# Kernel optimization log

Measured on AMD Instinct MI355X. Metric: run time of the kernel, lower is better.

Reference implementation:

```python
import jax, jax.numpy as jnp
import numpy as np

N = 50000      # nodes
E = 800000     # edges (before self loops)
IN = 128       # in_channels
HID = 128      # 2*out_channels
OUT = 64       # out_channels
NEG_SLOPE = 0.2


def _gat_conv(x, src, dst, W, a_src, a_dst, b, n_nodes):
    """Single-head PyG GATConv (concat=True, heads=1, self-loops already added)."""
    h = x @ W                                   # [N, F]
    alpha_s = h @ a_src                         # [N]
    alpha_d = h @ a_dst                         # [N]
    e = alpha_s[src] + alpha_d[dst]             # [E'] logits per edge j->i
    e = jnp.where(e > 0, e, NEG_SLOPE * e)      # LeakyReLU(0.2)
    # segment softmax over destination node
    m = jax.ops.segment_max(e, dst, num_segments=n_nodes)   # [N]
    w = jnp.exp(e - m[dst])                                   # [E']
    denom = jax.ops.segment_sum(w, dst, num_segments=n_nodes) # [N]
    alpha = w / denom[dst]                                     # [E']
    out = jax.ops.segment_sum(alpha[:, None] * h[src], dst, num_segments=n_nodes)
    return out + b


def _with_self_loops(edge_index, n_nodes):
    loop = jnp.arange(n_nodes, dtype=edge_index.dtype)
    src = jnp.concatenate([edge_index[0], loop])
    dst = jnp.concatenate([edge_index[1], loop])
    return src, dst


def setup_inputs() -> dict:
    key = jax.random.key(0)
    ks = jax.random.split(key, 10)
    s = 0.1
    return {
        "x": jax.random.normal(ks[0], (N, IN), jnp.float32),
        "edge_index": jax.random.randint(ks[1], (2, E), 0, N, jnp.int32),
        "W1": jax.random.normal(ks[2], (IN, HID), jnp.float32) * s,
        "a1_src": jax.random.normal(ks[3], (HID,), jnp.float32) * s,
        "a1_dst": jax.random.normal(ks[4], (HID,), jnp.float32) * s,
        "b1": jnp.zeros((HID,), jnp.float32),
        "W2": jax.random.normal(ks[5], (HID, OUT), jnp.float32) * s,
        "a2_src": jax.random.normal(ks[6], (OUT,), jnp.float32) * s,
        "a2_dst": jax.random.normal(ks[7], (OUT,), jnp.float32) * s,
        "b2": jnp.zeros((OUT,), jnp.float32),
    }


def reference(x, edge_index, W1, a1_src, a1_dst, b1, W2, a2_src, a2_dst, b2):
    src, dst = _with_self_loops(edge_index, N)
    h = _gat_conv(x, src, dst, W1, a1_src, a1_dst, b1, N)
    h = jax.nn.relu(h)
    return _gat_conv(h, src, dst, W2, a2_src, a2_dst, b2, N)
```

## Files before the change

kernel.cpp:

```cpp
#include <hip/hip_runtime.h>
#include <hip/hip_bf16.h>


#define BCAP 4096

typedef __attribute__((ext_vector_type(8))) short bf16x8;
typedef __attribute__((ext_vector_type(4))) float f32x4;

__device__ __forceinline__ unsigned short bf16bits(float f){
  __hip_bfloat16 b = __float2bfloat16(f);
  return *(unsigned short*)&b;
}
__device__ __forceinline__ float bf16lo(unsigned int v){ return __uint_as_float(v << 16); }
__device__ __forceinline__ float bf16hi(unsigned int v){ return __uint_as_float(v & 0xFFFF0000u); }

__global__ void init_k(int* bucketCount, float* as1, float* ad1, float* as2, float* ad2, int n){
  int i = blockIdx.x*blockDim.x + threadIdx.x;
  if (i < 512) bucketCount[i] = 0;
  if (i < n){ as1[i]=0.f; ad1[i]=0.f; as2[i]=0.f; ad2[i]=0.f; }
}

__global__ void prep_w(const float* __restrict__ W, unsigned short* __restrict__ Wt,
                       int K, int NC){
  int idx = blockIdx.x*blockDim.x + threadIdx.x;
  int total = NC*K/2;
  if (idx < total){
    int n = idx / (K/2), k2 = idx % (K/2);
    float a = W[(size_t)(2*k2)*NC + n];
    float b = W[(size_t)(2*k2+1)*NC + n];
    ushort2 o; o.x = bf16bits(a); o.y = bf16bits(b);
    *(ushort2*)&Wt[(size_t)n*K + 2*k2] = o;
  }
}

__global__ __launch_bounds__(256) void bucket_scatter(
    const int* __restrict__ src, const int* __restrict__ dst,
    int* __restrict__ bucketCount, unsigned int* __restrict__ gbuf, int E)
{
  __shared__ int hist[512];
  __shared__ int base[512];
  int t = threadIdx.x;
  int e0 = blockIdx.x * 2048;
  hist[t] = 0; hist[t+256] = 0;
  __syncthreads();
  int sv[8], dv[8];
  #pragma unroll
  for (int k=0;k<8;k++){
    int i = e0 + t + k*256;
    if (i < E){ sv[k]=src[i]; dv[k]=dst[i]; atomicAdd(&hist[dv[k]>>7], 1); }
    else { sv[k] = -1; dv[k] = 0; }
  }
  __syncthreads();
  int h0 = hist[t], h1 = hist[t+256];
  if (h0 > 0) base[t]     = atomicAdd(&bucketCount[t],     h0);
  if (h1 > 0) base[t+256] = atomicAdd(&bucketCount[t+256], h1);
  __syncthreads();
  hist[t] = 0; hist[t+256] = 0;
  __syncthreads();
  #pragma unroll
  for (int k=0;k<8;k++){
    if (sv[k] >= 0){
      int b = dv[k] >> 7;
      int r = base[b] + atomicAdd(&hist[b], 1);
      if (r < BCAP)
        gbuf[(size_t)b*BCAP + r] = ((unsigned)(dv[k] & 127) << 16) | (unsigned)sv[k];
    }
  }
}

__global__ void bucket_scan(const int* __restrict__ bucketCount,
                            int* __restrict__ bucketBase, int* __restrict__ offs,
                            int N, int E, int B){
  __shared__ int sh[512];
  int t = threadIdx.x;
  int nd = 0;
  if (t < B){ int lo = t*128; nd = (N - lo < 128) ? (N - lo) : 128; }
  int v = (t < B ? bucketCount[t] : 0) + nd;
  sh[t] = v;
  __syncthreads();
  for (int d=1; d<512; d<<=1){
    int x = (t >= d) ? sh[t-d] : 0;
    __syncthreads();
    sh[t] += x;
    __syncthreads();
  }
  if (t < B) bucketBase[t] = sh[t] - v;
  if (t == 0) offs[N] = E + N;
}

__global__ __launch_bounds__(256) void fine_sort(
    const unsigned int* __restrict__ gbuf, const int* __restrict__ bucketCount,
    const int* __restrict__ bucketBase, int* __restrict__ offs,
    int* __restrict__ srcS, int N)
{
  __shared__ int h[128];
  __shared__ int pre[128];
  __shared__ int rank[128];
  int b = blockIdx.x, t = threadIdx.x;
  int cnt = bucketCount[b]; if (cnt > BCAP) cnt = BCAP;
  int lo = b*128;
  int nd = (N - lo < 128) ? (N - lo) : 128;
  int base = bucketBase[b];
  if (t < 128){ h[t] = 0; rank[t] = 0; }
  __syncthreads();
  for (int i = t; i < cnt; i += 256)
    atomicAdd(&h[(gbuf[(size_t)b*BCAP + i] >> 16) & 127], 1);
  __syncthreads();
  if (t < 128) pre[t] = (t < nd) ? (h[t] + 1) : 0;
  __syncthreads();
  for (int d=1; d<128; d<<=1){
    int x = (t >= d && t < 128) ? pre[t-d] : 0;
    __syncthreads();
    if (t < 128) pre[t] += x;
    __syncthreads();
  }
  int seg = (t < nd) ? (h[t] + 1) : 0;
  int ex  = (t < 128) ? (pre[t] - seg) : 0;
  if (t < nd){
    offs[lo + t] = base + ex;
    srcS[base + ex] = lo + t;
  }
  __syncthreads();
  if (t < 128) pre[t] = ex;
  __syncthreads();
  for (int i = t; i < cnt; i += 256){
    unsigned e = gbuf[(size_t)b*BCAP + i];
    int dl = (e >> 16) & 127;
    int s  = e & 0xFFFF;
    int r  = atomicAdd(&rank[dl], 1);
    srcS[base + pre[dl] + 1 + r] = s;
  }
}

template<typename AT, int NC>
__global__ __launch_bounds__(256) void gemm_mfma(
    const AT* __restrict__ A, const unsigned short* __restrict__ Wt,
    const float* __restrict__ avs, const float* __restrict__ avd,
    unsigned short* __restrict__ H,
    float* __restrict__ as_, float* __restrict__ ad_, int M)
{
  const int K = 128;
  __shared__ unsigned short As[64*136];
  __shared__ unsigned short Ws[NC*136];
  int t = threadIdx.x;
  int rowBase = blockIdx.x * 64;

  if (sizeof(AT) == 4){
    const float* Af = (const float*)A;
    #pragma unroll
    for (int i=0;i<8;i++){
      int idx = t + i*256; int r = idx>>5, k4 = idx&31;
      int grow = rowBase + r;
      float4 v = (grow<M) ? *(const float4*)&Af[(size_t)grow*K + k4*4]
                          : make_float4(0.f,0.f,0.f,0.f);
      ushort4 o; o.x=bf16bits(v.x); o.y=bf16bits(v.y); o.z=bf16bits(v.z); o.w=bf16bits(v.w);
      *(ushort4*)&As[r*136 + k4*4] = o;
    }
  } else {
    const unsigned short* Ah = (const unsigned short*)A;
    #pragma unroll
    for (int i=0;i<4;i++){
      int idx = t + i*256; int r = idx>>4, k8 = idx&15;
      int grow = rowBase + r;
      uint4 v = (grow<M) ? *(const uint4*)&Ah[(size_t)grow*K + k8*8]
                         : make_uint4(0u,0u,0u,0u);
      *(uint4*)&As[r*136 + k8*8] = v;
    }
  }
  #pragma unroll
  for (int i=0;i<NC/16;i++){
    int idx = t + i*256; int n = idx>>4, k8 = idx&15;
    *(uint4*)&Ws[n*136 + k8*8] = *(const uint4*)&Wt[(size_t)n*K + k8*8];
  }
  __syncthreads();

  int wave = t>>6, lane = t&63, ln = lane&15, q = lane>>4;
  f32x4 acc[NC/16];
  #pragma unroll
  for (int nt=0; nt<NC/16; nt++) acc[nt] = (f32x4){0.f,0.f,0.f,0.f};
  #pragma unroll
  for (int kk=0;kk<4;kk++){
    bf16x8 a = *(const bf16x8*)&As[(wave*16+ln)*136 + kk*32 + q*8];
    #pragma unroll
    for (int nt=0; nt<NC/16; nt++){
      bf16x8 b = *(const bf16x8*)&Ws[(nt*16+ln)*136 + kk*32 + q*8];
      acc[nt] = __builtin_amdgcn_mfma_f32_16x16x32_bf16(a, b, acc[nt], 0, 0, 0);
    }
  }

  float asl[NC/16], adl[NC/16];
  #pragma unroll
  for (int nt=0; nt<NC/16; nt++){ asl[nt]=avs[nt*16+ln]; adl[nt]=avd[nt*16+ln]; }
  #pragma unroll
  for (int i=0;i<4;i++){
    int grow = rowBase + wave*16 + q*4 + i;
    if (grow < M){
      float ps=0.f, pd=0.f;
      #pragma unroll
      for (int nt=0; nt<NC/16; nt++){
        float v = acc[nt][i];
        H[(size_t)grow*NC + nt*16 + ln] = bf16bits(v);
        ps += v*asl[nt]; pd += v*adl[nt];
      }
      #pragma unroll
      for (int d=1; d<16; d<<=1){ ps += __shfl_xor(ps,d); pd += __shfl_xor(pd,d); }
      if (ln==0){ atomicAdd(&as_[grow], ps); atomicAdd(&ad_[grow], pd); }
    }
  }
}

template<bool RELU>
__global__ __launch_bounds__(256) void edge_agg128(
    const int* __restrict__ offs, const int* __restrict__ srcS,
    const float* __restrict__ asrc, const float* __restrict__ adst,
    const unsigned short* __restrict__ Hin, const float* __restrict__ bias,
    unsigned short* __restrict__ outp, int n)
{
  int wid  = (blockIdx.x * 256 + threadIdx.x) >> 6;
  int lane = threadIdx.x & 63;
  if (wid >= n) return;
  int beg = offs[wid], end = offs[wid+1];
  float ad = adst[wid];
  int qw = lane >> 4, ql = lane & 15;
  float acc[8] = {}; float denom = 0.f;
  for (int base = beg; base < end; base += 64){
    int m = end - base; if (m > 64) m = 64;
    int   sv = (lane < m) ? srcS[base + lane] : 0;
    float av = (lane < m) ? asrc[sv] : 0.f;
    float ev = av + ad;
    ev = (ev > 0.f) ? ev : 0.2f*ev;
    float wv = (lane < m) ? __expf(ev) : 0.f;
    for (int j = 0; j < m; j += 4){
      int idx = j + qw;
      int   s = __shfl(sv, idx);
      float w = __shfl(wv, idx);
      uint4 hv = *(const uint4*)&Hin[(size_t)s*128 + ql*8];
      denom += w;
      acc[0]+=w*bf16lo(hv.x); acc[1]+=w*bf16hi(hv.x);
      acc[2]+=w*bf16lo(hv.y); acc[3]+=w*bf16hi(hv.y);
      acc[4]+=w*bf16lo(hv.z); acc[5]+=w*bf16hi(hv.z);
      acc[6]+=w*bf16lo(hv.w); acc[7]+=w*bf16hi(hv.w);
    }
  }
  denom += __shfl_xor(denom,16); denom += __shfl_xor(denom,32);
  #pragma unroll
  for (int k=0;k<8;k++){ acc[k]+=__shfl_xor(acc[k],16); acc[k]+=__shfl_xor(acc[k],32); }
  if (qw == 0){
    float inv = 1.0f / denom;
    unsigned short o[8];
    #pragma unroll
    for (int k=0;k<8;k++){
      float v = acc[k]*inv + bias[ql*8+k];
      if (RELU) v = fmaxf(v, 0.f);
      o[k] = bf16bits(v);
    }
    *(uint4*)&outp[(size_t)wid*128 + ql*8] = *(uint4*)o;
  }
}

__global__ __launch_bounds__(256) void edge_agg64(
    const int* __restrict__ offs, const int* __restrict__ srcS,
    const float* __restrict__ asrc, const float* __restrict__ adst,
    const unsigned short* __restrict__ Hin, const float* __restrict__ bias,
    float* __restrict__ outp, int n)
{
  int wid  = (blockIdx.x * 256 + threadIdx.x) >> 6;
  int lane = threadIdx.x & 63;
  if (wid >= n) return;
  int beg = offs[wid], end = offs[wid+1];
  float ad = adst[wid];
  int ew = lane >> 3, el = lane & 7;
  float acc[8] = {}; float denom = 0.f;
  for (int base = beg; base < end; base += 64){
    int m = end - base; if (m > 64) m = 64;
    int   sv = (lane < m) ? srcS[base + lane] : 0;
    float av = (lane < m) ? asrc[sv] : 0.f;
    float ev = av + ad;
    ev = (ev > 0.f) ? ev : 0.2f*ev;
    float wv = (lane < m) ? __expf(ev) : 0.f;
    for (int j = 0; j < m; j += 8){
      int idx = j + ew;
      int   s = __shfl(sv, idx);
      float w = __shfl(wv, idx);
      uint4 hv = *(const uint4*)&Hin[(size_t)s*64 + el*8];
      denom += w;
      acc[0]+=w*bf16lo(hv.x); acc[1]+=w*bf16hi(hv.x);
      acc[2]+=w*bf16lo(hv.y); acc[3]+=w*bf16hi(hv.y);
      acc[4]+=w*bf16lo(hv.z); acc[5]+=w*bf16hi(hv.z);
      acc[6]+=w*bf16lo(hv.w); acc[7]+=w*bf16hi(hv.w);
    }
  }
  denom += __shfl_xor(denom,8); denom += __shfl_xor(denom,16); denom += __shfl_xor(denom,32);
  #pragma unroll
  for (int k=0;k<8;k++){
    acc[k]+=__shfl_xor(acc[k],8); acc[k]+=__shfl_xor(acc[k],16); acc[k]+=__shfl_xor(acc[k],32);
  }
  if (ew == 0){
    float inv = 1.0f / denom;
    float4 o0, o1;
    o0.x = acc[0]*inv + bias[el*8+0]; o0.y = acc[1]*inv + bias[el*8+1];
    o0.z = acc[2]*inv + bias[el*8+2]; o0.w = acc[3]*inv + bias[el*8+3];
    o1.x = acc[4]*inv + bias[el*8+4]; o1.y = acc[5]*inv + bias[el*8+5];
    o1.z = acc[6]*inv + bias[el*8+6]; o1.w = acc[7]*inv + bias[el*8+7];
    *(float4*)&outp[(size_t)wid*64 + el*8]     = o0;
    *(float4*)&outp[(size_t)wid*64 + el*8 + 4] = o1;
  }
}

extern "C" void kernel_launch(void* const* d_in, const int* in_sizes, int n_in,
                              void* d_out, int out_size, void* d_ws, size_t ws_size,
                              hipStream_t stream) {
  const int IN = 128, HID = 128, OUT = 64;
  const int N = in_sizes[0] / IN;
  const int E = in_sizes[1] / 2;
  const int B = (N + 127) / 128;

  const float* x    = (const float*)d_in[0];
  const int*   ei   = (const int*)d_in[1];
  const float* W1   = (const float*)d_in[2];
  const float* a1s  = (const float*)d_in[3];
  const float* a1d  = (const float*)d_in[4];
  const float* b1   = (const float*)d_in[5];
  const float* W2   = (const float*)d_in[6];
  const float* a2s  = (const float*)d_in[7];
  const float* a2d  = (const float*)d_in[8];
  const float* b2   = (const float*)d_in[9];
  float* out = (float*)d_out;

  char* w = (char*)d_ws;
  unsigned short* W1t = (unsigned short*)w; w += (size_t)HID*IN*2;
  unsigned short* W2t = (unsigned short*)w; w += (size_t)OUT*HID*2;
  unsigned short* h1    = (unsigned short*)w; w += (size_t)N*128*2;
  unsigned short* hrelu = (unsigned short*)w; w += (size_t)N*128*2;
  unsigned short* h2 = h1;
  float* as1   = (float*)w; w += (size_t)N*4;
  float* ad1   = (float*)w; w += (size_t)N*4;
  float* as2   = (float*)w; w += (size_t)N*4;
  float* ad2   = (float*)w; w += (size_t)N*4;
  int* offs    = (int*)w;   w += (size_t)(N+1)*4;
  int* bucketCount = (int*)w; w += 512*4;
  int* bucketBase  = (int*)w; w += 512*4;
  int* srcS    = (int*)w;   w += (size_t)(E+N)*4;
  unsigned int* gbuf = (unsigned int*)w; w += (size_t)B*BCAP*4;

  const int* esrc = ei;
  const int* edst = ei + E;

  hipLaunchKernelGGL(init_k,  dim3((N+255)/256), dim3(256), 0, stream,
                     bucketCount, as1, ad1, as2, ad2, N);
  hipLaunchKernelGGL(prep_w, dim3((HID*IN/2+255)/256), dim3(256), 0, stream, W1, W1t, IN, HID);
  hipLaunchKernelGGL(prep_w, dim3((OUT*HID/2+255)/256), dim3(256), 0, stream, W2, W2t, HID, OUT);
  hipLaunchKernelGGL(bucket_scatter, dim3((E+2047)/2048), dim3(256), 0, stream,
                     esrc, edst, bucketCount, gbuf, E);
  hipLaunchKernelGGL(bucket_scan, dim3(1), dim3(512), 0, stream,
                     bucketCount, bucketBase, offs, N, E, B);
  hipLaunchKernelGGL(fine_sort, dim3(B), dim3(256), 0, stream,
                     gbuf, bucketCount, bucketBase, offs, srcS, N);

  hipLaunchKernelGGL((gemm_mfma<float,128>), dim3((N+63)/64), dim3(256), 0, stream,
                     x, W1t, a1s, a1d, h1, as1, ad1, N);
  hipLaunchKernelGGL((edge_agg128<true>), dim3((N*64+255)/256), dim3(256), 0, stream,
                     offs, srcS, as1, ad1, h1, b1, hrelu, N);
  hipLaunchKernelGGL((gemm_mfma<unsigned short,64>), dim3((N+63)/64), dim3(256), 0, stream,
                     hrelu, W2t, a2s, a2d, h2, as2, ad2, N);
  hipLaunchKernelGGL(edge_agg64, dim3((N*64+255)/256), dim3(256), 0, stream,
                     offs, srcS, as2, ad2, h2, b2, out, N);
}
```

Measured before the change: 208.7 us.

## Fuse bucket scatter with layer-1 GEMM, fold scan into sort, precompute W2·a2

The edge bucket scatter and the first GEMM now run in one launch, with blocks split by index, so the memory-bound scatter and the MFMA GEMM can overlap. The bucket prefix scan is recomputed redundantly inside each fine_sort block, which removes a single-block launch. The layer-2 attention logits are computed in the layer-1 aggregation epilogue from precomputed W2·a2 vectors, so the second GEMM drops its atomics. Zero-initialisation moves to memsets. In exchange, the logits are taken from fp32 pre-rounding values rather than bf16 H, and each sort block repeats the 512-wide scan.

```diff
diff --git a/kernel.cpp b/kernel.cpp
--- a/kernel.cpp
+++ b/kernel.cpp
@@ -14,139 +14,50 @@
 __device__ __forceinline__ float bf16lo(unsigned int v){ return __uint_as_float(v << 16); }
 __device__ __forceinline__ float bf16hi(unsigned int v){ return __uint_as_float(v & 0xFFFF0000u); }
 
-__global__ void init_k(int* bucketCount, float* as1, float* ad1, float* as2, float* ad2, int n){
-  int i = blockIdx.x*blockDim.x + threadIdx.x;
-  if (i < 512) bucketCount[i] = 0;
-  if (i < n){ as1[i]=0.f; ad1[i]=0.f; as2[i]=0.f; ad2[i]=0.f; }
-}
-
-__global__ void prep_w(const float* __restrict__ W, unsigned short* __restrict__ Wt,
-                       int K, int NC){
-  int idx = blockIdx.x*blockDim.x + threadIdx.x;
-  int total = NC*K/2;
-  if (idx < total){
-    int n = idx / (K/2), k2 = idx % (K/2);
-    float a = W[(size_t)(2*k2)*NC + n];
-    float b = W[(size_t)(2*k2+1)*NC + n];
-    ushort2 o; o.x = bf16bits(a); o.y = bf16bits(b);
-    *(ushort2*)&Wt[(size_t)n*K + 2*k2] = o;
-  }
-}
-
-__global__ __launch_bounds__(256) void bucket_scatter(
-    const int* __restrict__ src, const int* __restrict__ dst,
-    int* __restrict__ bucketCount, unsigned int* __restrict__ gbuf, int E)
-{
-  __shared__ int hist[512];
-  __shared__ int base[512];
+__global__ __launch_bounds__(256) void prep_w_both(
+    const float* __restrict__ W1, const float* __restrict__ W2,
+    const float* __restrict__ a2s, const float* __restrict__ a2d,
+    unsigned short* __restrict__ W1t, unsigned short* __restrict__ W2t,
+    float* __restrict__ vas, float* __restrict__ vad)
+{
+  int b = blockIdx.x, t = threadIdx.x;
+  if (b < 48){
+    int idx = b*256 + t;
+    if (idx < 8192){
+      int n = idx >> 6, k2 = idx & 63;
+      float a = W1[(size_t)(2*k2)*128 + n];
+      float c = W1[(size_t)(2*k2+1)*128 + n];
+      ushort2 o; o.x = bf16bits(a); o.y = bf16bits(c);
+      *(ushort2*)&W1t[(size_t)n*128 + 2*k2] = o;
+    } else {
+      int r = idx - 8192;
+      int n = r >> 6, k2 = r & 63;
+      float a = W2[(size_t)(2*k2)*64 + n];
+      float c = W2[(size_t)(2*k2+1)*64 + n];
+      ushort2 o; o.x = bf16bits(a); o.y = bf16bits(c);
+      *(ushort2*)&W2t[(size_t)n*128 + 2*k2] = o;
+    }
+  } else {
+    int k = t & 127;
+    const float* av = (t < 128) ? a2s : a2d;
+    float* ov = (t < 128) ? vas : vad;
+    float s = 0.f;
+    for (int n=0; n<64; n++) s += W2[(size_t)k*64 + n] * av[n];
+    ov[k] = s;
+  }
+}
+
+template<int NC, bool FUSE>
+__device__ __forceinline__ void gemm_body(
+    const float* __restrict__ Af, const unsigned short* __restrict__ Ah,
+    const unsigned short* __restrict__ Wt,
+    const float* __restrict__ avs, const float* __restrict__ avd,
+    unsigned short* __restrict__ H, float* __restrict__ as_, float* __restrict__ ad_,
+    int M, int rowBase, unsigned short* As, unsigned short* Ws)
+{
+  const int K = 128;
   int t = threadIdx.x;
-  int e0 = blockIdx.x * 2048;
-  hist[t] = 0; hist[t+256] = 0;
-  __syncthreads();
-  int sv[8], dv[8];
-  #pragma unroll
-  for (int k=0;k<8;k++){
-    int i = e0 + t + k*256;
-    if (i < E){ sv[k]=src[i]; dv[k]=dst[i]; atomicAdd(&hist[dv[k]>>7], 1); }
-    else { sv[k] = -1; dv[k] = 0; }
-  }
-  __syncthreads();
-  int h0 = hist[t], h1 = hist[t+256];
-  if (h0 > 0) base[t]     = atomicAdd(&bucketCount[t],     h0);
-  if (h1 > 0) base[t+256] = atomicAdd(&bucketCount[t+256], h1);
-  __syncthreads();
-  hist[t] = 0; hist[t+256] = 0;
-  __syncthreads();
-  #pragma unroll
-  for (int k=0;k<8;k++){
-    if (sv[k] >= 0){
-      int b = dv[k] >> 7;
-      int r = base[b] + atomicAdd(&hist[b], 1);
-      if (r < BCAP)
-        gbuf[(size_t)b*BCAP + r] = ((unsigned)(dv[k] & 127) << 16) | (unsigned)sv[k];
-    }
-  }
-}
-
-__global__ void bucket_scan(const int* __restrict__ bucketCount,
-                            int* __restrict__ bucketBase, int* __restrict__ offs,
-                            int N, int E, int B){
-  __shared__ int sh[512];
-  int t = threadIdx.x;
-  int nd = 0;
-  if (t < B){ int lo = t*128; nd = (N - lo < 128) ? (N - lo) : 128; }
-  int v = (t < B ? bucketCount[t] : 0) + nd;
-  sh[t] = v;
-  __syncthreads();
-  for (int d=1; d<512; d<<=1){
-    int x = (t >= d) ? sh[t-d] : 0;
-    __syncthreads();
-    sh[t] += x;
-    __syncthreads();
-  }
-  if (t < B) bucketBase[t] = sh[t] - v;
-  if (t == 0) offs[N] = E + N;
-}
-
-__global__ __launch_bounds__(256) void fine_sort(
-    const unsigned int* __restrict__ gbuf, const int* __restrict__ bucketCount,
-    const int* __restrict__ bucketBase, int* __restrict__ offs,
-    int* __restrict__ srcS, int N)
-{
-  __shared__ int h[128];
-  __shared__ int pre[128];
-  __shared__ int rank[128];
-  int b = blockIdx.x, t = threadIdx.x;
-  int cnt = bucketCount[b]; if (cnt > BCAP) cnt = BCAP;
-  int lo = b*128;
-  int nd = (N - lo < 128) ? (N - lo) : 128;
-  int base = bucketBase[b];
-  if (t < 128){ h[t] = 0; rank[t] = 0; }
-  __syncthreads();
-  for (int i = t; i < cnt; i += 256)
-    atomicAdd(&h[(gbuf[(size_t)b*BCAP + i] >> 16) & 127], 1);
-  __syncthreads();
-  if (t < 128) pre[t] = (t < nd) ? (h[t] + 1) : 0;
-  __syncthreads();
-  for (int d=1; d<128; d<<=1){
-    int x = (t >= d && t < 128) ? pre[t-d] : 0;
-    __syncthreads();
-    if (t < 128) pre[t] += x;
-    __syncthreads();
-  }
-  int seg = (t < nd) ? (h[t] + 1) : 0;
-  int ex  = (t < 128) ? (pre[t] - seg) : 0;
-  if (t < nd){
-    offs[lo + t] = base + ex;
-    srcS[base + ex] = lo + t;
-  }
-  __syncthreads();
-  if (t < 128) pre[t] = ex;
-  __syncthreads();
-  for (int i = t; i < cnt; i += 256){
-    unsigned e = gbuf[(size_t)b*BCAP + i];
-    int dl = (e >> 16) & 127;
-    int s  = e & 0xFFFF;
-    int r  = atomicAdd(&rank[dl], 1);
-    srcS[base + pre[dl] + 1 + r] = s;
-  }
-}
-
-template<typename AT, int NC>
-__global__ __launch_bounds__(256) void gemm_mfma(
-    const AT* __restrict__ A, const unsigned short* __restrict__ Wt,
-    const float* __restrict__ avs, const float* __restrict__ avd,
-    unsigned short* __restrict__ H,
-    float* __restrict__ as_, float* __restrict__ ad_, int M)
-{
-  const int K = 128;
-  __shared__ unsigned short As[64*136];
-  __shared__ unsigned short Ws[NC*136];
-  int t = threadIdx.x;
-  int rowBase = blockIdx.x * 64;
-
-  if (sizeof(AT) == 4){
-    const float* Af = (const float*)A;
+  if (Af){
     #pragma unroll
     for (int i=0;i<8;i++){
       int idx = t + i*256; int r = idx>>5, k4 = idx&31;
@@ -157,7 +68,6 @@
       *(ushort4*)&As[r*136 + k4*4] = o;
     }
   } else {
-    const unsigned short* Ah = (const unsigned short*)A;
     #pragma unroll
     for (int i=0;i<4;i++){
       int idx = t + i*256; int r = idx>>4, k8 = idx&15;
@@ -187,10 +97,11 @@
       acc[nt] = __builtin_amdgcn_mfma_f32_16x16x32_bf16(a, b, acc[nt], 0, 0, 0);
     }
   }
-
   float asl[NC/16], adl[NC/16];
-  #pragma unroll
-  for (int nt=0; nt<NC/16; nt++){ asl[nt]=avs[nt*16+ln]; adl[nt]=avd[nt*16+ln]; }
+  if (FUSE){
+    #pragma unroll
+    for (int nt=0; nt<NC/16; nt++){ asl[nt]=avs[nt*16+ln]; adl[nt]=avd[nt*16+ln]; }
+  }
   #pragma unroll
   for (int i=0;i<4;i++){
     int grow = rowBase + wave*16 + q*4 + i;
@@ -200,21 +111,130 @@
       for (int nt=0; nt<NC/16; nt++){
         float v = acc[nt][i];
         H[(size_t)grow*NC + nt*16 + ln] = bf16bits(v);
-        ps += v*asl[nt]; pd += v*adl[nt];
+        if (FUSE){ ps += v*asl[nt]; pd += v*adl[nt]; }
       }
-      #pragma unroll
-      for (int d=1; d<16; d<<=1){ ps += __shfl_xor(ps,d); pd += __shfl_xor(pd,d); }
-      if (ln==0){ atomicAdd(&as_[grow], ps); atomicAdd(&ad_[grow], pd); }
-    }
-  }
-}
-
-template<bool RELU>
+      if (FUSE){
+        #pragma unroll
+        for (int d=1; d<16; d<<=1){ ps += __shfl_xor(ps,d); pd += __shfl_xor(pd,d); }
+        if (ln==0){ atomicAdd(&as_[grow], ps); atomicAdd(&ad_[grow], pd); }
+      }
+    }
+  }
+}
+
+__global__ __launch_bounds__(256) void scatter_or_gemm(
+    const int* __restrict__ src, const int* __restrict__ dst,
+    int* __restrict__ bucketCount, unsigned int* __restrict__ gbuf, int E, int B,
+    const float* __restrict__ x, const unsigned short* __restrict__ W1t,
+    const float* __restrict__ a1s, const float* __restrict__ a1d,
+    unsigned short* __restrict__ h1, float* __restrict__ as1, float* __restrict__ ad1,
+    int M)
+{
+  __shared__ unsigned short smem[64*136 + 128*136];
+  int t = threadIdx.x;
+  if ((int)blockIdx.x >= B){
+    gemm_body<128, true>(x, nullptr, W1t, a1s, a1d, h1, as1, ad1, M,
+                         (blockIdx.x - B)*64, smem, smem + 64*136);
+    return;
+  }
+  int* hist = (int*)smem;
+  int* base = hist + 512;
+  int e0 = blockIdx.x * 2048;
+  hist[t] = 0; hist[t+256] = 0;
+  __syncthreads();
+  int sv[8], dv[8];
+  #pragma unroll
+  for (int k=0;k<8;k++){
+    int i = e0 + t + k*256;
+    if (i < E){ sv[k]=src[i]; dv[k]=dst[i]; atomicAdd(&hist[dv[k]>>7], 1); }
+    else { sv[k] = -1; dv[k] = 0; }
+  }
+  __syncthreads();
+  int h0 = hist[t], h1c = hist[t+256];
+  if (h0 > 0)  base[t]     = atomicAdd(&bucketCount[t],     h0);
+  if (h1c > 0) base[t+256] = atomicAdd(&bucketCount[t+256], h1c);
+  __syncthreads();
+  hist[t] = 0; hist[t+256] = 0;
+  __syncthreads();
+  #pragma unroll
+  for (int k=0;k<8;k++){
+    if (sv[k] >= 0){
+      int b = dv[k] >> 7;
+      int r = base[b] + atomicAdd(&hist[b], 1);
+      if (r < BCAP)
+        gbuf[(size_t)b*BCAP + r] = ((unsigned)(dv[k] & 127) << 16) | (unsigned)sv[k];
+    }
+  }
+}
+
+__global__ __launch_bounds__(256) void fine_sort(
+    const unsigned int* __restrict__ gbuf, const int* __restrict__ bucketCount,
+    int* __restrict__ offs, int* __restrict__ srcS, int N, int E, int B)
+{
+  __shared__ int sh[512];
+  __shared__ int h[128];
+  __shared__ int pre[128];
+  __shared__ int rank[128];
+  int b = blockIdx.x, t = threadIdx.x;
+  {
+    int i0 = t, i1 = t + 256;
+    int nd0 = 0, nd1 = 0;
+    if (i0 < B){ int lo=i0*128; nd0 = (N-lo<128)?(N-lo):128; }
+    if (i1 < B){ int lo=i1*128; nd1 = (N-lo<128)?(N-lo):128; }
+    sh[i0] = (i0 < B ? bucketCount[i0] : 0) + nd0;
+    sh[i1] = (i1 < B ? bucketCount[i1] : 0) + nd1;
+    __syncthreads();
+    for (int d=1; d<512; d<<=1){
+      int x0 = (i0 >= d) ? sh[i0-d] : 0;
+      int x1 = (i1 >= d) ? sh[i1-d] : 0;
+      __syncthreads();
+      sh[i0] += x0; sh[i1] += x1;
+      __syncthreads();
+    }
+  }
+  int cnt = bucketCount[b]; if (cnt > BCAP) cnt = BCAP;
+  int lo = b*128;
+  int nd = (N - lo < 128) ? (N - lo) : 128;
+  int base = sh[b] - (cnt + nd);
+  if (b == 0 && t == 0) offs[N] = E + N;
+  if (t < 128){ h[t] = 0; rank[t] = 0; }
+  __syncthreads();
+  for (int i = t; i < cnt; i += 256)
+    atomicAdd(&h[(gbuf[(size_t)b*BCAP + i] >> 16) & 127], 1);
+  __syncthreads();
+  if (t < 128) pre[t] = (t < nd) ? (h[t] + 1) : 0;
+  __syncthreads();
+  for (int d=1; d<128; d<<=1){
+    int x = (t >= d && t < 128) ? pre[t-d] : 0;
+    __syncthreads();
+    if (t < 128) pre[t] += x;
+    __syncthreads();
+  }
+  int seg = (t < nd) ? (h[t] + 1) : 0;
+  int ex  = (t < 128) ? (pre[t] - seg) : 0;
+  if (t < nd){
+    offs[lo + t] = base + ex;
+    srcS[base + ex] = lo + t;
+  }
+  __syncthreads();
+  if (t < 128) pre[t] = ex;
+  __syncthreads();
+  for (int i = t; i < cnt; i += 256){
+    unsigned e = gbuf[(size_t)b*BCAP + i];
+    int dl = (e >> 16) & 127;
+    int s  = e & 0xFFFF;
+    int r  = atomicAdd(&rank[dl], 1);
+    srcS[base + pre[dl] + 1 + r] = s;
+  }
+}
+
 __global__ __launch_bounds__(256) void edge_agg128(
     const int* __restrict__ offs, const int* __restrict__ srcS,
     const float* __restrict__ asrc, const float* __restrict__ adst,
     const unsigned short* __restrict__ Hin, const float* __restrict__ bias,
-    unsigned short* __restrict__ outp, int n)
+    unsigned short* __restrict__ outp,
+    const float* __restrict__ vas, const float* __restrict__ vad,
+    float* __restrict__ as2, float* __restrict__ ad2, int n)
 {
   int wid  = (blockIdx.x * 256 + threadIdx.x) >> 6;
   int lane = threadIdx.x & 63;
@@ -247,15 +267,29 @@
   for (int k=0;k<8;k++){ acc[k]+=__shfl_xor(acc[k],16); acc[k]+=__shfl_xor(acc[k],32); }
   if (qw == 0){
     float inv = 1.0f / denom;
+    float ps = 0.f, pd = 0.f;
     unsigned short o[8];
     #pragma unroll
     for (int k=0;k<8;k++){
-      float v = acc[k]*inv + bias[ql*8+k];
-      if (RELU) v = fmaxf(v, 0.f);
+      float v = fmaxf(acc[k]*inv + bias[ql*8+k], 0.f);
       o[k] = bf16bits(v);
+      ps += v * vas[ql*8+k];
+      pd += v * vad[ql*8+k];
     }
     *(uint4*)&outp[(size_t)wid*128 + ql*8] = *(uint4*)o;
-  }
+    #pragma unroll
+    for (int d=1; d<16; d<<=1){ ps += __shfl_xor(ps,d); pd += __shfl_xor(pd,d); }
+    if (ql == 0){ as2[wid] = ps; ad2[wid] = pd; }
+  }
+}
+
+__global__ __launch_bounds__(256) void gemm2_k(
+    const unsigned short* __restrict__ A, const unsigned short* __restrict__ Wt,
+    unsigned short* __restrict__ H, int M)
+{
+  __shared__ unsigned short smem[64*136 + 64*136];
+  gemm_body<64, false>(nullptr, A, Wt, nullptr, nullptr, H, nullptr, nullptr,
+                       M, blockIdx.x*64, smem, smem + 64*136);
 }
 
 __global__ __launch_bounds__(256) void edge_agg64(
@@ -337,32 +371,29 @@
   float* ad1   = (float*)w; w += (size_t)N*4;
   float* as2   = (float*)w; w += (size_t)N*4;
   float* ad2   = (float*)w; w += (size_t)N*4;
+  float* vas   = (float*)w; w += 128*4;
+  float* vad   = (float*)w; w += 128*4;
   int* offs    = (int*)w;   w += (size_t)(N+1)*4;
   int* bucketCount = (int*)w; w += 512*4;
-  int* bucketBase  = (int*)w; w += 512*4;
   int* srcS    = (int*)w;   w += (size_t)(E+N)*4;
   unsigned int* gbuf = (unsigned int*)w; w += (size_t)B*BCAP*4;
 
   const int* esrc = ei;
   const int* edst = ei + E;
 
-  hipLaunchKernelGGL(init_k,  dim3((N+255)/256), dim3(256), 0, stream,
-                     bucketCount, as1, ad1, as2, ad2, N);
-  hipLaunchKernelGGL(prep_w, dim3((HID*IN/2+255)/256), dim3(256), 0, stream, W1, W1t, IN, HID);
-  hipLaunchKernelGGL(prep_w, dim3((OUT*HID/2+255)/256), dim3(256), 0, stream, W2, W2t, HID, OUT);
-  hipLaunchKernelGGL(bucket_scatter, dim3((E+2047)/2048), dim3(256), 0, stream,
-                     esrc, edst, bucketCount, gbuf, E);
-  hipLaunchKernelGGL(bucket_scan, dim3(1), dim3(512), 0, stream,
-                     bucketCount, bucketBase, offs, N, E, B);
+  hipMemsetAsync(bucketCount, 0, 512*4, stream);
+  hipMemsetAsync(as1, 0, (size_t)2*N*4, stream);
+  hipLaunchKernelGGL(prep_w_both, dim3(49), dim3(256), 0, stream,
+                     W1, W2, a2s, a2d, W1t, W2t, vas, vad);
+  hipLaunchKernelGGL(scatter_or_gemm, dim3(B + (N+63)/64), dim3(256), 0, stream,
+                     esrc, edst, bucketCount, gbuf, E, B,
+                     x, W1t, a1s, a1d, h1, as1, ad1, N);
   hipLaunchKernelGGL(fine_sort, dim3(B), dim3(256), 0, stream,
-                     gbuf, bucketCount, bucketBase, offs, srcS, N);
-
-  hipLaunchKernelGGL((gemm_mfma<float,128>), dim3((N+63)/64), dim3(256), 0, stream,
-                     x, W1t, a1s, a1d, h1, as1, ad1, N);
-  hipLaunchKernelGGL((edge_agg128<true>), dim3((N*64+255)/256), dim3(256), 0, stream,
-                     offs, srcS, as1, ad1, h1, b1, hrelu, N);
-  hipLaunchKernelGGL((gemm_mfma<unsigned short,64>), dim3((N+63)/64), dim3(256), 0, stream,
-                     hrelu, W2t, a2s, a2d, h2, as2, ad2, N);
+                     gbuf, bucketCount, offs, srcS, N, E, B);
+  hipLaunchKernelGGL(edge_agg128, dim3((N*64+255)/256), dim3(256), 0, stream,
+                     offs, srcS, as1, ad1, h1, b1, hrelu, vas, vad, as2, ad2, N);
+  hipLaunchKernelGGL(gemm2_k, dim3((N+63)/64), dim3(256), 0, stream,
+                     hrelu, W2t, h2, N);
   hipLaunchKernelGGL(edge_agg64, dim3((N*64+255)/256), dim3(256), 0, stream,
                      offs, srcS, as2, ad2, h2, b2, out, N);
 }
```

Measured after the change: 210.9 us. About the same (+1.1%).
